# Kernel tuning notes

Measured on AMD Instinct MI355X. Metric: run time of the kernel, lower is better.

## Reference

```python
import jax, jax.numpy as jnp
import numpy as np

K = 64          # number of tags, incl. BOS/EOS
V = 50000       # vocab size (excl. BOS/EOS words)
D = 128         # lexicon embedding dim
BOS_T = K - 2   # BOS tag index
EOS_T = K - 1   # EOS tag index
BATCH = 8192
L = 126         # interior words per sentence (n = L + 2 incl. BOS/EOS)
EPS = 1e-45     # smoothing added to A and B in updateAB


def setup_inputs() -> dict:
    key = jax.random.key(0)
    k1, k2, k3, k4 = jax.random.split(key, 4)
    words = jax.random.randint(k1, (BATCH, L), 0, V, dtype=jnp.int32)
    ThetaB = 0.01 * jax.random.uniform(k2, (K, D), dtype=jnp.float32)
    WA = 0.01 * jax.random.uniform(k3, (K, K), dtype=jnp.float32)
    E = jax.random.normal(k4, (V, D), dtype=jnp.float32)
    return {"words": words, "ThetaB": ThetaB, "WA": WA, "E": E}


def reference(words, ThetaB, WA, E):
    # updateAB(): A = softmax(WA) with BOS column forced to prob 0 (-inf logit)
    WAm = WA.at[:, BOS_T].set(-jnp.inf)
    A = jax.nn.softmax(WAm, axis=1) + EPS                       # [K, K]
    B = jax.nn.softmax(ThetaB @ E.T, axis=1)                    # [K, V]
    B = B.at[EOS_T, :].set(0.0).at[BOS_T, :].set(0.0) + EPS
    logA = jnp.log(A)                                           # [K, K]
    logB = jnp.log(B)                                           # [K, V]

    # Emission log-probs gathered per token: [L, B, K]
    em = jnp.swapaxes(logB.T[words], 0, 1)

    # alpha_0: one-hot (in log space) at BOS tag
    alpha0 = jnp.full((words.shape[0], K), -jnp.inf, dtype=logA.dtype)
    alpha0 = alpha0.at[:, BOS_T].set(0.0)

    def step(alpha, e):
        # alpha: [B, K] over prev tags; logsumexp over prev tag axis
        new = jax.nn.logsumexp(alpha[:, :, None] + logA[None, :, :], axis=1) + e
        return new, None

    alpha, _ = jax.lax.scan(step, alpha0, em)
    # Final transition into EOS tag (no emission): log Z per sentence, [B]
    logZ = jax.nn.logsumexp(alpha + logA[None, :, EOS_T], axis=1)
    return logZ
```

## Files before the change

kernel.cpp:

```cpp
#include <hip/hip_runtime.h>
#include <hip/hip_bf16.h>
#include <math.h>


#define KT 64
#define VV 50000
#define DD 128
#define BOS_T 62
#define EOS_T 63
#define LLEN 126
#define EPSF 1e-45f
#define SCALE_F 65536.0f
#define LOG_TOTAL_SCALE (2016.0f * 0.6931471805599453f)
#define NBLK 782
#define PBLK 784

#define BTN_OFF   0
#define A_OFF     6400000
#define SUM_OFF   6416384
#define PART_OFF  6416640

typedef short short8 __attribute__((ext_vector_type(8)));
typedef float f32x4  __attribute__((ext_vector_type(4)));

union U8 { short8 v; unsigned u[4]; short s[8]; };

static __device__ inline unsigned short f2bf_u(float x) {
    __hip_bfloat16 h = __float2bfloat16(x);
    return *reinterpret_cast<unsigned short*>(&h);
}
static __device__ inline short f2bf(float x) { return (short)f2bf_u(x); }

#if __has_builtin(__builtin_amdgcn_cvt_pk_bf16_f32)
typedef __bf16 bf16x2 __attribute__((ext_vector_type(2)));
static __device__ inline unsigned pk2(float a, float b) {
    bf16x2 r = __builtin_amdgcn_cvt_pk_bf16_f32(a, b);
    return *reinterpret_cast<unsigned*>(&r);
}
#else
static __device__ inline unsigned pk2(float a, float b) {
    union { float f; unsigned u; } ua, ub;
    ua.f = a; ub.f = b;
    return ((ua.u + 0x8000u) >> 16) | ((ub.u + 0x8000u) & 0xFFFF0000u);
}
#endif
static __device__ inline float lo16(unsigned u) { union { unsigned i; float f; } c; c.i = u << 16;        return c.f; }
static __device__ inline float hi16(unsigned u) { union { unsigned i; float f; } c; c.i = u & 0xffff0000u; return c.f; }

__global__ __launch_bounds__(256) void k_emit(const float* __restrict__ ThetaB,
                                              const float* __restrict__ E,
                                              unsigned short* __restrict__ btn_bf,
                                              float* __restrict__ partial) {
    __shared__ float red[4][KT];
    int t    = threadIdx.x;
    int lane = t & 63;
    int w    = t >> 6;
    int n    = lane & 15;
    int q    = lane >> 4;
    int v0   = (blockIdx.x * 4 + w) * 16;

    int rowE = v0 + n; rowE = rowE < VV ? rowE : VV - 1;
    float4 ex[4][2];
#pragma unroll
    for (int kt = 0; kt < 4; ++kt) {
        const float* p = E + (size_t)rowE * DD + kt * 32 + q * 8;
        ex[kt][0] = *(const float4*)p;
        ex[kt][1] = *(const float4*)(p + 4);
    }

    short8 Bf[4][4];
#pragma unroll
    for (int kt = 0; kt < 4; ++kt)
#pragma unroll
        for (int nt = 0; nt < 4; ++nt) {
            const float* p = ThetaB + (nt * 16 + n) * DD + kt * 32 + q * 8;
            float4 x = *(const float4*)p;
            float4 y = *(const float4*)(p + 4);
            U8 f;
            f.u[0] = pk2(x.x, x.y); f.u[1] = pk2(x.z, x.w);
            f.u[2] = pk2(y.x, y.y); f.u[3] = pk2(y.z, y.w);
            Bf[kt][nt] = f.v;
        }

    short8 Ae[4];
#pragma unroll
    for (int kt = 0; kt < 4; ++kt) {
        U8 f;
        f.u[0] = pk2(ex[kt][0].x, ex[kt][0].y); f.u[1] = pk2(ex[kt][0].z, ex[kt][0].w);
        f.u[2] = pk2(ex[kt][1].x, ex[kt][1].y); f.u[3] = pk2(ex[kt][1].z, ex[kt][1].w);
        Ae[kt] = f.v;
    }

#pragma unroll
    for (int nt = 0; nt < 4; ++nt) {
        f32x4 C = {0.f, 0.f, 0.f, 0.f};
#pragma unroll
        for (int kt = 0; kt < 4; ++kt)
            C = __builtin_amdgcn_mfma_f32_16x16x32_bf16(Ae[kt], Bf[kt][nt], C, 0, 0, 0);
        float ps = 0.0f;
#pragma unroll
        for (int r = 0; r < 4; ++r) {
            int row = v0 + 4 * q + r;
            float e = __expf(C[r]);
            if (row < VV) {
                btn_bf[(size_t)row * KT + nt * 16 + n] = f2bf_u(e);
                ps += e;
            }
        }
        ps += __shfl_xor(ps, 16, 64);
        ps += __shfl_xor(ps, 32, 64);
        if (q == 0) red[w][nt * 16 + n] = ps;
    }
    __syncthreads();
    if (w == 0) {
        float s = red[0][lane] + red[1][lane] + red[2][lane] + red[3][lane];
        partial[lane * PBLK + blockIdx.x] = s;
    }
}

__global__ __launch_bounds__(256) void k_sumA(const float* __restrict__ partial,
                                              const float* __restrict__ WA,
                                              float* __restrict__ sumexp,
                                              float* __restrict__ A) {
    __shared__ float r[4];
    int k = blockIdx.x;
    int t = threadIdx.x;
    float s = 0.0f;
    for (int i = t; i < NBLK; i += 256) s += partial[k * PBLK + i];
#pragma unroll
    for (int off = 32; off > 0; off >>= 1) s += __shfl_xor(s, off, 64);
    if ((t & 63) == 0) r[t >> 6] = s;
    __syncthreads();
    if (t == 0) sumexp[k] = r[0] + r[1] + r[2] + r[3];
    if (t < 64) {
        float wv = WA[k * KT + t];
        float e = (t == BOS_T) ? 0.0f : __expf(wv);
        float se = e;
#pragma unroll
        for (int off = 32; off > 0; off >>= 1) se += __shfl_xor(se, off, 64);
        A[k * KT + t] = e / se + EPSF;
    }
}

__global__ __launch_bounds__(64) void k_fwd(const int* __restrict__ words,
                                            const unsigned short* __restrict__ btn_bf,
                                            const float* __restrict__ A,
                                            const float* __restrict__ sumexp,
                                            float* __restrict__ out) {
    __shared__ int shw[16 * LLEN];
    int lane = threadIdx.x & 63;
    int n    = lane & 15;
    int qA   = lane >> 4;
    int b0   = blockIdx.x * 16;

    {
        const uint4* src = (const uint4*)(words + (size_t)b0 * LLEN);
        uint4* dst = (uint4*)shw;
#pragma unroll
        for (int i = 0; i < 8; ++i) {
            int idx = lane + 64 * i;
            if (idx < (16 * LLEN) / 4) dst[idx] = src[idx];
        }
    }

    short8 Af[2][4];
#pragma unroll
    for (int mt = 0; mt < 4; ++mt) {
        int tagn = 32 * (mt >> 1) + 8 * (n >> 2) + 4 * (mt & 1) + (n & 3);
        float s = sumexp[tagn];
        float rsn = (tagn == BOS_T || tagn == EOS_T) ? 0.0f : (SCALE_F / s);
#pragma unroll
        for (int kt = 0; kt < 2; ++kt) {
            U8 f;
#pragma unroll
            for (int j = 0; j < 8; ++j)
                f.s[j] = f2bf(A[(kt * 32 + qA * 8 + j) * KT + tagn] * rsn);
            Af[kt][mt] = f.v;
        }
    }

    short8 B0, B1;
    {
        U8 z; z.u[0] = z.u[1] = z.u[2] = z.u[3] = 0;
        B0 = z.v;
        U8 o; o.u[0] = o.u[1] = o.u[2] = o.u[3] = 0;
        if (qA == 3) o.s[6] = (short)0x3F80;
        B1 = o.v;
    }

    const int* wrow = shw + n * LLEN;

    uint4 ep0[6], ep1[6];
#pragma unroll
    for (int d = 0; d < 6; ++d) {
        int wd = wrow[d];
        ep0[d] = *(const uint4*)(btn_bf + (size_t)wd * KT + qA * 8);
        ep1[d] = *(const uint4*)(btn_bf + (size_t)wd * KT + 32 + qA * 8);
    }
    int w1 = wrow[6], w2 = wrow[7];

    for (int l6 = 0; l6 < LLEN; l6 += 6) {
#pragma unroll
        for (int u = 0; u < 6; ++u) {
            int g = l6 + u;
            uint4 e0 = ep0[u], e1 = ep1[u];
            {
                int wg = w1; w1 = w2;
                int wi = g + 8; wi = wi < LLEN ? wi : LLEN - 1;
                w2 = wrow[wi];
                ep0[u] = *(const uint4*)(btn_bf + (size_t)wg * KT + qA * 8);
                ep1[u] = *(const uint4*)(btn_bf + (size_t)wg * KT + 32 + qA * 8);
            }
            f32x4 C[4];
#pragma unroll
            for (int mt = 0; mt < 4; ++mt) {
                f32x4 acc = {0.f, 0.f, 0.f, 0.f};
                acc = __builtin_amdgcn_mfma_f32_16x16x32_bf16(Af[0][mt], B0, acc, 0, 0, 0);
                acc = __builtin_amdgcn_mfma_f32_16x16x32_bf16(Af[1][mt], B1, acc, 0, 0, 0);
                C[mt] = acc;
            }
            U8 f0, f1;
            f0.u[0] = pk2(C[0][0] * lo16(e0.x), C[0][1] * hi16(e0.x));
            f0.u[1] = pk2(C[0][2] * lo16(e0.y), C[0][3] * hi16(e0.y));
            f0.u[2] = pk2(C[1][0] * lo16(e0.z), C[1][1] * hi16(e0.z));
            f0.u[3] = pk2(C[1][2] * lo16(e0.w), C[1][3] * hi16(e0.w));
            f1.u[0] = pk2(C[2][0] * lo16(e1.x), C[2][1] * hi16(e1.x));
            f1.u[1] = pk2(C[2][2] * lo16(e1.y), C[2][3] * hi16(e1.y));
            f1.u[2] = pk2(C[3][0] * lo16(e1.z), C[3][1] * hi16(e1.z));
            f1.u[3] = pk2(C[3][2] * lo16(e1.w), C[3][3] * hi16(e1.w));
            B0 = f0.v; B1 = f1.v;
        }
    }

    short8 Afin[2];
#pragma unroll
    for (int kt = 0; kt < 2; ++kt) {
        U8 f;
#pragma unroll
        for (int j = 0; j < 8; ++j)
            f.s[j] = (n == 0) ? f2bf(A[(kt * 32 + qA * 8 + j) * KT + EOS_T]) : (short)0;
        Afin[kt] = f.v;
    }
    f32x4 Cf = {0.f, 0.f, 0.f, 0.f};
    Cf = __builtin_amdgcn_mfma_f32_16x16x32_bf16(Afin[0], B0, Cf, 0, 0, 0);
    Cf = __builtin_amdgcn_mfma_f32_16x16x32_bf16(Afin[1], B1, Cf, 0, 0, 0);
    if (qA == 0)
        out[b0 + n] = logf(Cf[0]) - LOG_TOTAL_SCALE;
}

extern "C" void kernel_launch(void* const* d_in, const int* in_sizes, int n_in,
                              void* d_out, int out_size, void* d_ws, size_t ws_size,
                              hipStream_t stream) {
    const int*   words  = (const int*)d_in[0];
    const float* ThetaB = (const float*)d_in[1];
    const float* WA     = (const float*)d_in[2];
    const float* E      = (const float*)d_in[3];
    float* out = (float*)d_out;

    char* ws = (char*)d_ws;
    unsigned short* btn_bf = (unsigned short*)(ws + BTN_OFF);
    float* A       = (float*)(ws + A_OFF);
    float* sumexp  = (float*)(ws + SUM_OFF);
    float* partial = (float*)(ws + PART_OFF);

    k_emit<<<NBLK, 256, 0, stream>>>(ThetaB, E, btn_bf, partial);
    k_sumA<<<KT, 256, 0, stream>>>(partial, WA, sumexp, A);
    k_fwd<<<8192 / 16, 64, 0, stream>>>(words, btn_bf, A, sumexp, out);
}
```

Measured before the change: 137.8 us.

## Double-buffer emission gathers through LDS with async global-to-LDS loads

The forward recursion kernel no longer prefetches emission rows into registers six steps ahead. It now stages 14 timesteps of gathered emission rows into a double-buffered LDS array using global_load_lds, overlapping the next phase's gathers with the current phase's MFMA recursion. Separately, the emission kernel swaps MFMA operand roles so each lane writes packed 4-element bf16 stores instead of scalar stores, and reduces partial sums along the other axis. This aims to hide gather latency and cut store count, at the cost of extra LDS use and full vmcnt waits at each phase boundary.

Result: no change. 139.4 us (+1.1%).

```diff
diff --git a/kernel.cpp b/kernel.cpp
--- a/kernel.cpp
+++ b/kernel.cpp
@@ -14,6 +14,8 @@
 #define LOG_TOTAL_SCALE (2016.0f * 0.6931471805599453f)
 #define NBLK 782
 #define PBLK 784
+#define TPH 14
+#define NPH 9
 
 #define BTN_OFF   0
 #define A_OFF     6400000
@@ -46,6 +48,17 @@
 #endif
 static __device__ inline float lo16(unsigned u) { union { unsigned i; float f; } c; c.i = u << 16;        return c.f; }
 static __device__ inline float hi16(unsigned u) { union { unsigned i; float f; } c; c.i = u & 0xffff0000u; return c.f; }
+
+#if __has_builtin(__builtin_amdgcn_global_load_lds)
+#define GLLDS(gp, lbase)                                                        \
+    __builtin_amdgcn_global_load_lds(                                           \
+        (__attribute__((address_space(1))) void*)const_cast<unsigned short*>(gp),\
+        (__attribute__((address_space(3))) void*)(lbase), 16, 0, 0)
+#else
+#define GLLDS(gp, lbase)                                                        \
+    do { *(uint4*)((unsigned short*)(lbase) + (threadIdx.x & 63) * 8) =         \
+             *(const uint4*)(gp); } while (0)
+#endif
 
 __global__ __launch_bounds__(256) void k_emit(const float* __restrict__ ThetaB,
                                               const float* __restrict__ E,
@@ -59,7 +72,9 @@
     int q    = lane >> 4;
     int v0   = (blockIdx.x * 4 + w) * 16;
 
-    int rowE = v0 + n; rowE = rowE < VV ? rowE : VV - 1;
+    int rowE = v0 + n;
+    bool valid = rowE < VV;
+    rowE = valid ? rowE : VV - 1;
     float4 ex[4][2];
 #pragma unroll
     for (int kt = 0; kt < 4; ++kt) {
@@ -68,48 +83,51 @@
         ex[kt][1] = *(const float4*)(p + 4);
     }
 
-    short8 Bf[4][4];
+    short8 Th[4][4];
 #pragma unroll
     for (int kt = 0; kt < 4; ++kt)
 #pragma unroll
-        for (int nt = 0; nt < 4; ++nt) {
-            const float* p = ThetaB + (nt * 16 + n) * DD + kt * 32 + q * 8;
+        for (int mt = 0; mt < 4; ++mt) {
+            const float* p = ThetaB + (mt * 16 + n) * DD + kt * 32 + q * 8;
             float4 x = *(const float4*)p;
             float4 y = *(const float4*)(p + 4);
             U8 f;
             f.u[0] = pk2(x.x, x.y); f.u[1] = pk2(x.z, x.w);
             f.u[2] = pk2(y.x, y.y); f.u[3] = pk2(y.z, y.w);
-            Bf[kt][nt] = f.v;
-        }
-
-    short8 Ae[4];
+            Th[kt][mt] = f.v;
+        }
+
+    short8 Ef[4];
 #pragma unroll
     for (int kt = 0; kt < 4; ++kt) {
         U8 f;
         f.u[0] = pk2(ex[kt][0].x, ex[kt][0].y); f.u[1] = pk2(ex[kt][0].z, ex[kt][0].w);
         f.u[2] = pk2(ex[kt][1].x, ex[kt][1].y); f.u[3] = pk2(ex[kt][1].z, ex[kt][1].w);
-        Ae[kt] = f.v;
-    }
-
-#pragma unroll
-    for (int nt = 0; nt < 4; ++nt) {
+        Ef[kt] = f.v;
+    }
+
+#pragma unroll
+    for (int mt = 0; mt < 4; ++mt) {
         f32x4 C = {0.f, 0.f, 0.f, 0.f};
 #pragma unroll
         for (int kt = 0; kt < 4; ++kt)
-            C = __builtin_amdgcn_mfma_f32_16x16x32_bf16(Ae[kt], Bf[kt][nt], C, 0, 0, 0);
-        float ps = 0.0f;
+            C = __builtin_amdgcn_mfma_f32_16x16x32_bf16(Th[kt][mt], Ef[kt], C, 0, 0, 0);
+        float e[4];
+#pragma unroll
+        for (int r = 0; r < 4; ++r) e[r] = __expf(C[r]);
+        if (valid) {
+            uint2 st = make_uint2(pk2(e[0], e[1]), pk2(e[2], e[3]));
+            *(uint2*)(btn_bf + (size_t)rowE * KT + mt * 16 + q * 4) = st;
+        }
 #pragma unroll
         for (int r = 0; r < 4; ++r) {
-            int row = v0 + 4 * q + r;
-            float e = __expf(C[r]);
-            if (row < VV) {
-                btn_bf[(size_t)row * KT + nt * 16 + n] = f2bf_u(e);
-                ps += e;
-            }
-        }
-        ps += __shfl_xor(ps, 16, 64);
-        ps += __shfl_xor(ps, 32, 64);
-        if (q == 0) red[w][nt * 16 + n] = ps;
+            float s = valid ? e[r] : 0.0f;
+            s += __shfl_xor(s, 1, 64);
+            s += __shfl_xor(s, 2, 64);
+            s += __shfl_xor(s, 4, 64);
+            s += __shfl_xor(s, 8, 64);
+            if (n == 0) red[w][mt * 16 + q * 4 + r] = s;
+        }
     }
     __syncthreads();
     if (w == 0) {
@@ -148,6 +166,7 @@
                                             const float* __restrict__ sumexp,
                                             float* __restrict__ out) {
     __shared__ int shw[16 * LLEN];
+    __shared__ __attribute__((aligned(16))) unsigned short shE[2][TPH * 1024];
     int lane = threadIdx.x & 63;
     int n    = lane & 15;
     int qA   = lane >> 4;
@@ -188,29 +207,35 @@
         B1 = o.v;
     }
 
-    const int* wrow = shw + n * LLEN;
-
-    uint4 ep0[6], ep1[6];
-#pragma unroll
-    for (int d = 0; d < 6; ++d) {
-        int wd = wrow[d];
-        ep0[d] = *(const uint4*)(btn_bf + (size_t)wd * KT + qA * 8);
-        ep1[d] = *(const uint4*)(btn_bf + (size_t)wd * KT + 32 + qA * 8);
-    }
-    int w1 = wrow[6], w2 = wrow[7];
-
-    for (int l6 = 0; l6 < LLEN; l6 += 6) {
-#pragma unroll
-        for (int u = 0; u < 6; ++u) {
-            int g = l6 + u;
-            uint4 e0 = ep0[u], e1 = ep1[u];
-            {
-                int wg = w1; w1 = w2;
-                int wi = g + 8; wi = wi < LLEN ? wi : LLEN - 1;
-                w2 = wrow[wi];
-                ep0[u] = *(const uint4*)(btn_bf + (size_t)wg * KT + qA * 8);
-                ep1[u] = *(const uint4*)(btn_bf + (size_t)wg * KT + 32 + qA * 8);
-            }
+#define STAGE(bb, t0)                                                        \
+    do {                                                                     \
+        _Pragma("unroll")                                                    \
+        for (int s_ = 0; s_ < TPH; ++s_) {                                   \
+            int wd_ = shw[n * LLEN + (t0) + s_];                             \
+            const unsigned short* g_ = btn_bf + (size_t)wd_ * KT + qA * 8;   \
+            GLLDS(g_, &shE[bb][s_ * 1024]);                                  \
+            GLLDS(g_ + 32, &shE[bb][s_ * 1024 + 512]);                       \
+        }                                                                    \
+    } while (0)
+
+#define LDE(bb, ss, hh) (*(const uint4*)(&shE[bb][(ss) * 1024 + (hh) * 512] + lane * 8))
+
+    STAGE(0, 0);
+    asm volatile("s_waitcnt vmcnt(0)" ::: "memory");
+
+    for (int p = 0; p < NPH; ++p) {
+        int b = p & 1;
+        if (p + 1 < NPH) STAGE((p + 1) & 1, (p + 1) * TPH);
+
+        uint4 a0 = LDE(b, 0, 0), a1 = LDE(b, 0, 1);
+        uint4 c0 = LDE(b, 1, 0), c1 = LDE(b, 1, 1);
+#pragma unroll
+        for (int s = 0; s < TPH; ++s) {
+            uint4 e0 = a0, e1 = a1;
+            a0 = c0; a1 = c1;
+            int s2 = (s + 2 < TPH) ? s + 2 : TPH - 1;
+            c0 = LDE(b, s2, 0); c1 = LDE(b, s2, 1);
+
             f32x4 C[4];
 #pragma unroll
             for (int mt = 0; mt < 4; ++mt) {
@@ -230,6 +255,7 @@
             f1.u[3] = pk2(C[3][2] * lo16(e1.w), C[3][3] * hi16(e1.w));
             B0 = f0.v; B1 = f1.v;
         }
+        asm volatile("s_waitcnt vmcnt(0)" ::: "memory");
     }
 
     short8 Afin[2];
```
